# Optimization experiments

Measured on AMD Instinct MI355X. Metric: run time of the kernel, lower is better.

The kernel has to match this reference:

```python
import jax, jax.numpy as jnp
import numpy as np

N_NODES = 100000
N_EDGES = 1600000
NFEAT, NHID, NCLASS = 128, 64, 40
NLAYERS = 4
P = 2.0


def setup_inputs() -> dict:
    key = jax.random.key(0)
    ks = jax.random.split(key, 10)
    x = jax.random.normal(ks[0], (N_NODES, NFEAT), dtype=jnp.float32)
    edge_index = jax.random.randint(ks[1], (2, N_EDGES), 0, N_NODES, dtype=jnp.int32)
    s_in = 1.0 / np.sqrt(NFEAT)
    s_h = 1.0 / np.sqrt(NHID)
    return {
        "x": x,
        "edge_index": edge_index,
        "enc_W": jax.random.normal(ks[2], (NHID, NFEAT), dtype=jnp.float32) * s_in,
        "enc_b": jnp.zeros((NHID,), dtype=jnp.float32),
        "conv_W": jax.random.normal(ks[3], (NHID, NHID), dtype=jnp.float32) * s_h,
        "conv_b": jnp.zeros((NHID,), dtype=jnp.float32),
        "W_skip": jax.random.normal(ks[4], (NHID, NHID), dtype=jnp.float32) * s_h,
        "dec_W": jax.random.normal(ks[5], (NCLASS, NHID), dtype=jnp.float32) * s_h,
        "dec_b": jnp.zeros((NCLASS,), dtype=jnp.float32),
    }


def _gcn_conv(X, W, b, src, dst, n):
    # PyG GCNConv: add self-loops, symmetric normalization, then X @ W^T + b
    H = X @ W.T  # [n, nhid]
    ones = jnp.ones_like(dst, dtype=X.dtype)
    deg = jax.ops.segment_sum(ones, dst, num_segments=n)  # in-degree incl. self loops
    dinv = jnp.where(deg > 0, jax.lax.rsqrt(deg), 0.0)
    norm = dinv[src] * dinv[dst]  # [E+n]
    out = jax.ops.segment_sum(norm[:, None] * H[src], dst, num_segments=n)
    return out + b


def _gamma(X, row, col, n, p):
    # G2 gating: scatter-mean over edges of sum |X[row]-X[col]|^p, then tanh.
    # (conv_gg output in the original G2 is dead code and omitted.)
    diff = jnp.sum(jnp.abs(X[row] - X[col]) ** p, axis=-1)  # [E]
    s = jax.ops.segment_sum(diff, row, num_segments=n)
    cnt = jax.ops.segment_sum(jnp.ones_like(diff), row, num_segments=n)
    return jnp.tanh(s / jnp.maximum(cnt, 1.0))  # [n]


def reference(x, edge_index, enc_W, enc_b, conv_W, conv_b, W_skip, dec_W, dec_b):
    n = x.shape[0]
    row, col = edge_index[0], edge_index[1]
    # self-loop augmented edges for GCNConv
    loop = jnp.arange(n, dtype=edge_index.dtype)
    src_sl = jnp.concatenate([row, loop])
    dst_sl = jnp.concatenate([col, loop])

    X = jax.nn.relu(x @ enc_W.T + enc_b)  # [n, nhid]
    X_init = X
    skip_val = X_init @ W_skip.T  # constant across layers

    for _ in range(NLAYERS):
        X_agg = jax.nn.relu(_gcn_conv(X, conv_W, conv_b, src_sl, dst_sl, n))
        g = _gamma(X, row, col, n, P)[:, None]  # gamma_smooth == gamma_squash (dead convs)
        denom = 1.0 + g + g
        A = 1.0 / denom
        B = g / denom
        C = g / denom
        X = A * X + B * X_agg + C * skip_val

    return X @ dec_W.T + dec_b  # [n, nclass]
```

## Files before the change

### kernel.cpp

```cpp
#include <hip/hip_runtime.h>
#include <hip/hip_bf16.h>

#define NFEAT 128
#define NHID  64
#define NCLASS 40
#define NLAYERS 4


__global__ void count_rank_k(const int* __restrict__ ei, int E,
                             int* __restrict__ cnt_col, int* __restrict__ rank) {
    int t = blockIdx.x * blockDim.x + threadIdx.x;
    int base = t * 4;
    if (base >= E) return;
    if (base + 4 <= E) {
        int4 c4 = *reinterpret_cast<const int4*>(ei + E + base);
        int4 k4;
        k4.x = atomicAdd(&cnt_col[c4.x], 1);
        k4.y = atomicAdd(&cnt_col[c4.y], 1);
        k4.z = atomicAdd(&cnt_col[c4.z], 1);
        k4.w = atomicAdd(&cnt_col[c4.w], 1);
        *reinterpret_cast<int4*>(rank + base) = k4;
    } else {
        for (int e = base; e < E; ++e)
            rank[e] = atomicAdd(&cnt_col[ei[E + e]], 1);
    }
}

__global__ void scanA_k(const int* __restrict__ cnt, int* __restrict__ off,
                        int* __restrict__ bsum, float* __restrict__ dinv, int n) {
    __shared__ int t[1024];
    int i = blockIdx.x * 1024 + threadIdx.x;
    int x = (i < n) ? cnt[i] : 0;
    if (i < n) dinv[i] = 1.0f / sqrtf((float)(x + 1));
    t[threadIdx.x] = x;
    __syncthreads();
    for (int d = 1; d < 1024; d <<= 1) {
        int y = (threadIdx.x >= (unsigned)d) ? t[threadIdx.x - d] : 0;
        __syncthreads();
        t[threadIdx.x] += y;
        __syncthreads();
    }
    if (i < n) off[i] = t[threadIdx.x] - x;
    if (threadIdx.x == 1023) bsum[blockIdx.x] = t[1023];
}

__global__ void scanB_k(int* __restrict__ bsum, int nb) {
    __shared__ int t[1024];
    int x = (threadIdx.x < (unsigned)nb) ? bsum[threadIdx.x] : 0;
    t[threadIdx.x] = x;
    __syncthreads();
    for (int d = 1; d < 1024; d <<= 1) {
        int y = (threadIdx.x >= (unsigned)d) ? t[threadIdx.x - d] : 0;
        __syncthreads();
        t[threadIdx.x] += y;
        __syncthreads();
    }
    if (threadIdx.x < (unsigned)nb) bsum[threadIdx.x] = t[threadIdx.x] - x;
}

__global__ void scanC_k(int* __restrict__ off, const int* __restrict__ bsum,
                        float* __restrict__ gs, int n, int total) {
    int i = blockIdx.x * 1024 + threadIdx.x;
    if (i < n) {
        off[i] += bsum[blockIdx.x];
        gs[i] = 0.f;
    }
    if (i == 0) off[n] = total;
}

__global__ void scatter_k(const int* __restrict__ ei, int E,
                          const int* __restrict__ col_off, const int* __restrict__ rank,
                          int* __restrict__ cnt_row, int* __restrict__ csr) {
    int t = blockIdx.x * blockDim.x + threadIdx.x;
    int base = t * 8;
    if (base >= E) return;
    if (base + 8 <= E) {
        int4 rA = *reinterpret_cast<const int4*>(ei + base);
        int4 rB = *reinterpret_cast<const int4*>(ei + base + 4);
        int4 cA = *reinterpret_cast<const int4*>(ei + E + base);
        int4 cB = *reinterpret_cast<const int4*>(ei + E + base + 4);
        int4 kA = *reinterpret_cast<const int4*>(rank + base);
        int4 kB = *reinterpret_cast<const int4*>(rank + base + 4);
        atomicAdd(&cnt_row[rA.x], 1);
        atomicAdd(&cnt_row[rA.y], 1);
        atomicAdd(&cnt_row[rA.z], 1);
        atomicAdd(&cnt_row[rA.w], 1);
        atomicAdd(&cnt_row[rB.x], 1);
        atomicAdd(&cnt_row[rB.y], 1);
        atomicAdd(&cnt_row[rB.z], 1);
        atomicAdd(&cnt_row[rB.w], 1);
        csr[col_off[cA.x] + kA.x] = rA.x;
        csr[col_off[cA.y] + kA.y] = rA.y;
        csr[col_off[cA.z] + kA.z] = rA.z;
        csr[col_off[cA.w] + kA.w] = rA.w;
        csr[col_off[cB.x] + kB.x] = rB.x;
        csr[col_off[cB.y] + kB.y] = rB.y;
        csr[col_off[cB.z] + kB.z] = rB.z;
        csr[col_off[cB.w] + kB.w] = rB.w;
    } else {
        for (int e = base; e < E; ++e) {
            atomicAdd(&cnt_row[ei[e]], 1);
            csr[col_off[ei[E + e]] + rank[e]] = ei[e];
        }
    }
}


template<int K, int M, bool RELU, bool BIAS>
__global__ void dense_small_k(const float* __restrict__ A, const float* __restrict__ W,
                              const float* __restrict__ b, float* __restrict__ out, int n) {
    int v = blockIdx.x * blockDim.x + threadIdx.x;
    if (v >= n) return;
    float a[K];
    const float4* ap = reinterpret_cast<const float4*>(A + (size_t)v * K);
#pragma unroll
    for (int k = 0; k < K / 4; ++k) {
        float4 t = ap[k];
        a[4 * k + 0] = t.x; a[4 * k + 1] = t.y; a[4 * k + 2] = t.z; a[4 * k + 3] = t.w;
    }
    float4* op = reinterpret_cast<float4*>(out + (size_t)v * M);
#pragma unroll 1
    for (int m = 0; m < M; m += 4) {
        float acc0 = BIAS ? b[m + 0] : 0.f;
        float acc1 = BIAS ? b[m + 1] : 0.f;
        float acc2 = BIAS ? b[m + 2] : 0.f;
        float acc3 = BIAS ? b[m + 3] : 0.f;
#pragma unroll
        for (int k = 0; k < K; ++k) {
            float av = a[k];
            acc0 = fmaf(av, W[(m + 0) * K + k], acc0);
            acc1 = fmaf(av, W[(m + 1) * K + k], acc1);
            acc2 = fmaf(av, W[(m + 2) * K + k], acc2);
            acc3 = fmaf(av, W[(m + 3) * K + k], acc3);
        }
        if (RELU) {
            acc0 = fmaxf(acc0, 0.f); acc1 = fmaxf(acc1, 0.f);
            acc2 = fmaxf(acc2, 0.f); acc3 = fmaxf(acc3, 0.f);
        }
        float4 o; o.x = acc0; o.y = acc1; o.z = acc2; o.w = acc3;
        op[m >> 2] = o;
    }
}


template<int K, int M, int MC>
__global__ void dense_enc_k(const float* __restrict__ A, const float* __restrict__ W,
                            const float* __restrict__ b, float* __restrict__ out, int n) {
    int v = blockIdx.x * blockDim.x + threadIdx.x;
    if (v >= n) return;
    const float4* ap = reinterpret_cast<const float4*>(A + (size_t)v * K);
    float4* op = reinterpret_cast<float4*>(out + (size_t)v * M);
#pragma unroll 1
    for (int mc = 0; mc < M; mc += MC) {
        float acc[MC];
#pragma unroll
        for (int m = 0; m < MC; ++m) acc[m] = b[mc + m];
#pragma unroll 1
        for (int kb = 0; kb < K / 4; ++kb) {
            float4 a4 = ap[kb];
#pragma unroll
            for (int m = 0; m < MC; ++m) {
                const float* wr = W + (size_t)(mc + m) * K + kb * 4;
                acc[m] = fmaf(a4.x, wr[0], acc[m]);
                acc[m] = fmaf(a4.y, wr[1], acc[m]);
                acc[m] = fmaf(a4.z, wr[2], acc[m]);
                acc[m] = fmaf(a4.w, wr[3], acc[m]);
            }
        }
#pragma unroll
        for (int m = 0; m < MC; m += 4) {
            float4 o;
            o.x = fmaxf(acc[m + 0], 0.f);
            o.y = fmaxf(acc[m + 1], 0.f);
            o.z = fmaxf(acc[m + 2], 0.f);
            o.w = fmaxf(acc[m + 3], 0.f);
            op[(mc + m) >> 2] = o;
        }
    }
}

__global__ void gather_k(const float* __restrict__ X, const int* __restrict__ csr,
                         const int* __restrict__ col_off, const float* __restrict__ dinv,
                         float* __restrict__ pre, float* __restrict__ gs, int n) {
    int gid = (blockIdx.x * blockDim.x + threadIdx.x) >> 4;
    int ngrp = (gridDim.x * blockDim.x) >> 4;
    int sub = threadIdx.x & 15;

    for (int v = gid; v < n; v += ngrp) {
        float4 xv = reinterpret_cast<const float4*>(X + (size_t)v * NHID)[sub];
        int beg = col_off[v], end = col_off[v + 1];
        float4 acc = make_float4(0.f, 0.f, 0.f, 0.f);
        int e = beg;
        for (; e + 4 <= end; e += 4) {
            int s0 = csr[e], s1 = csr[e + 1], s2 = csr[e + 2], s3 = csr[e + 3];
            float w0 = dinv[s0], w1 = dinv[s1], w2 = dinv[s2], w3 = dinv[s3];
            float4 x0 = reinterpret_cast<const float4*>(X + (size_t)s0 * NHID)[sub];
            float4 x1 = reinterpret_cast<const float4*>(X + (size_t)s1 * NHID)[sub];
            float4 x2 = reinterpret_cast<const float4*>(X + (size_t)s2 * NHID)[sub];
            float4 x3 = reinterpret_cast<const float4*>(X + (size_t)s3 * NHID)[sub];
            acc.x = fmaf(w0, x0.x, acc.x); acc.y = fmaf(w0, x0.y, acc.y);
            acc.z = fmaf(w0, x0.z, acc.z); acc.w = fmaf(w0, x0.w, acc.w);
            acc.x = fmaf(w1, x1.x, acc.x); acc.y = fmaf(w1, x1.y, acc.y);
            acc.z = fmaf(w1, x1.z, acc.z); acc.w = fmaf(w1, x1.w, acc.w);
            acc.x = fmaf(w2, x2.x, acc.x); acc.y = fmaf(w2, x2.y, acc.y);
            acc.z = fmaf(w2, x2.z, acc.z); acc.w = fmaf(w2, x2.w, acc.w);
            acc.x = fmaf(w3, x3.x, acc.x); acc.y = fmaf(w3, x3.y, acc.y);
            acc.z = fmaf(w3, x3.z, acc.z); acc.w = fmaf(w3, x3.w, acc.w);
            float dx = x0.x - xv.x; float p0 = dx * dx;
            dx = x0.y - xv.y; p0 = fmaf(dx, dx, p0);
            dx = x0.z - xv.z; p0 = fmaf(dx, dx, p0);
            dx = x0.w - xv.w; p0 = fmaf(dx, dx, p0);
            dx = x1.x - xv.x; float p1 = dx * dx;
            dx = x1.y - xv.y; p1 = fmaf(dx, dx, p1);
            dx = x1.z - xv.z; p1 = fmaf(dx, dx, p1);
            dx = x1.w - xv.w; p1 = fmaf(dx, dx, p1);
            dx = x2.x - xv.x; float p2 = dx * dx;
            dx = x2.y - xv.y; p2 = fmaf(dx, dx, p2);
            dx = x2.z - xv.z; p2 = fmaf(dx, dx, p2);
            dx = x2.w - xv.w; p2 = fmaf(dx, dx, p2);
            dx = x3.x - xv.x; float p3 = dx * dx;
            dx = x3.y - xv.y; p3 = fmaf(dx, dx, p3);
            dx = x3.z - xv.z; p3 = fmaf(dx, dx, p3);
            dx = x3.w - xv.w; p3 = fmaf(dx, dx, p3);
#pragma unroll
            for (int m = 1; m <= 8; m <<= 1) {
                p0 += __shfl_xor(p0, m, 64);
                p1 += __shfl_xor(p1, m, 64);
                p2 += __shfl_xor(p2, m, 64);
                p3 += __shfl_xor(p3, m, 64);
            }
            if (sub == 0) {
                atomicAdd(&gs[s0], p0);
                atomicAdd(&gs[s1], p1);
                atomicAdd(&gs[s2], p2);
                atomicAdd(&gs[s3], p3);
            }
        }
        for (; e < end; ++e) {
            int s = csr[e];
            float w = dinv[s];
            float4 xs = reinterpret_cast<const float4*>(X + (size_t)s * NHID)[sub];
            acc.x = fmaf(w, xs.x, acc.x); acc.y = fmaf(w, xs.y, acc.y);
            acc.z = fmaf(w, xs.z, acc.z); acc.w = fmaf(w, xs.w, acc.w);
            float dx = xs.x - xv.x; float part = dx * dx;
            dx = xs.y - xv.y; part = fmaf(dx, dx, part);
            dx = xs.z - xv.z; part = fmaf(dx, dx, part);
            dx = xs.w - xv.w; part = fmaf(dx, dx, part);
#pragma unroll
            for (int m = 1; m <= 8; m <<= 1) part += __shfl_xor(part, m, 64);
            if (sub == 0) atomicAdd(&gs[s], part);
        }
        float dv = dinv[v];
        float dv2 = dv * dv;
        float4 o;
        o.x = fmaf(dv, acc.x, dv2 * xv.x);
        o.y = fmaf(dv, acc.y, dv2 * xv.y);
        o.z = fmaf(dv, acc.z, dv2 * xv.z);
        o.w = fmaf(dv, acc.w, dv2 * xv.w);
        reinterpret_cast<float4*>(pre + (size_t)v * NHID)[sub] = o;
    }
}

__global__ void update_k(float* __restrict__ X, const float* __restrict__ pre,
                         const float* __restrict__ skip, const float* __restrict__ W,
                         const float* __restrict__ b, float* __restrict__ gs,
                         const int* __restrict__ cnt_row, int n) {
    int v = blockIdx.x * blockDim.x + threadIdx.x;
    if (v >= n) return;
    float a[NHID];
    const float4* ap = reinterpret_cast<const float4*>(pre + (size_t)v * NHID);
#pragma unroll
    for (int k = 0; k < NHID / 4; ++k) {
        float4 t = ap[k];
        a[4 * k + 0] = t.x; a[4 * k + 1] = t.y; a[4 * k + 2] = t.z; a[4 * k + 3] = t.w;
    }
    float gv = tanhf(gs[v] / fmaxf((float)cnt_row[v], 1.f));
    gs[v] = 0.f;
    float inv = 1.0f / (1.0f + 2.0f * gv);

    float4* Xp = reinterpret_cast<float4*>(X + (size_t)v * NHID);
    const float4* Sp = reinterpret_cast<const float4*>(skip + (size_t)v * NHID);
#pragma unroll 1
    for (int m = 0; m < NHID; m += 4) {
        float t0 = b[m + 0], t1 = b[m + 1], t2 = b[m + 2], t3 = b[m + 3];
#pragma unroll
        for (int k = 0; k < NHID; ++k) {
            float av = a[k];
            t0 = fmaf(av, W[(m + 0) * NHID + k], t0);
            t1 = fmaf(av, W[(m + 1) * NHID + k], t1);
            t2 = fmaf(av, W[(m + 2) * NHID + k], t2);
            t3 = fmaf(av, W[(m + 3) * NHID + k], t3);
        }
        t0 = fmaxf(t0, 0.f); t1 = fmaxf(t1, 0.f);
        t2 = fmaxf(t2, 0.f); t3 = fmaxf(t3, 0.f);
        float4 x4 = Xp[m >> 2];
        float4 s4 = Sp[m >> 2];
        float4 o;
        o.x = (x4.x + gv * (t0 + s4.x)) * inv;
        o.y = (x4.y + gv * (t1 + s4.y)) * inv;
        o.z = (x4.z + gv * (t2 + s4.z)) * inv;
        o.w = (x4.w + gv * (t3 + s4.w)) * inv;
        Xp[m >> 2] = o;
    }
}


extern "C" void kernel_launch(void* const* d_in, const int* in_sizes, int n_in,
                              void* d_out, int out_size, void* d_ws, size_t ws_size,
                              hipStream_t stream) {
    const float* x      = (const float*)d_in[0];
    const int*   ei     = (const int*)  d_in[1];
    const float* enc_W  = (const float*)d_in[2];
    const float* enc_b  = (const float*)d_in[3];
    const float* conv_W = (const float*)d_in[4];
    const float* conv_b = (const float*)d_in[5];
    const float* W_skip = (const float*)d_in[6];
    const float* dec_W  = (const float*)d_in[7];
    const float* dec_b  = (const float*)d_in[8];

    const int n = in_sizes[0] / NFEAT;
    const int E = in_sizes[1] / 2;

    char* ws = (char*)d_ws;
    auto alloc = [&](size_t bytes) {
        char* p = ws;
        ws += (bytes + 255) & ~(size_t)255;
        return p;
    };

    float* X    = (float*)alloc((size_t)n * NHID * 4);
    float* pre  = (float*)alloc((size_t)n * NHID * 4);
    float* skip = (float*)alloc((size_t)n * NHID * 4);
    float* gs   = (float*)alloc((size_t)n * 4);
    float* dinv = (float*)alloc((size_t)n * 4);
    int* cnt_row = (int*)alloc((size_t)n * 4);
    int* cnt_col = (int*)alloc((size_t)n * 4);
    int* col_off = (int*)alloc((size_t)(n + 1) * 4);
    int* rank    = (int*)alloc((size_t)E * 4);
    int* bsc     = (int*)alloc(1024 * 4);
    int* csr     = (int*)alloc((size_t)E * 4);

    hipMemsetAsync(cnt_row, 0, (size_t)n * 4, stream);
    hipMemsetAsync(cnt_col, 0, (size_t)n * 4, stream);

    count_rank_k<<<(E / 4 + 255) / 256, 256, 0, stream>>>(ei, E, cnt_col, rank);

    int nb = (n + 1023) / 1024;
    scanA_k<<<nb, 1024, 0, stream>>>(cnt_col, col_off, bsc, dinv, n);
    scanB_k<<<1, 1024, 0, stream>>>(bsc, nb);
    scanC_k<<<nb, 1024, 0, stream>>>(col_off, bsc, gs, n, E);
    scatter_k<<<(E / 8 + 255) / 256, 256, 0, stream>>>(ei, E, col_off, rank, cnt_row, csr);

    dense_enc_k<NFEAT, NHID, 32><<<(n + 255) / 256, 256, 0, stream>>>(x, enc_W, enc_b, X, n);
    dense_small_k<NHID, NHID, false, false><<<(n + 255) / 256, 256, 0, stream>>>(X, W_skip, nullptr, skip, n);

    for (int l = 0; l < NLAYERS; ++l) {
        gather_k<<<2048, 256, 0, stream>>>(X, csr, col_off, dinv, pre, gs, n);
        update_k<<<(n + 255) / 256, 256, 0, stream>>>(X, pre, skip, conv_W, conv_b, gs, cnt_row, n);
    }

    dense_small_k<NHID, NCLASS, false, true><<<(n + 255) / 256, 256, 0, stream>>>(X, dec_W, dec_b, (float*)d_out, n);
}
```

Baseline: 994.2 us.

## Gather neighbor features from a bf16 shadow copy and fuse encoder with skip projection

Keeps a bf16 copy of the node features, written by the encoder and update kernels, and has the edge gather read that copy instead of the fp32 rows. This halves the bytes fetched per neighbor in the random-access gather, which is the dominant cost. The gather loop is unrolled to 8 edges, the encoder and skip projection are fused into one kernel, and launch bounds are added to all kernels. The trade-off is bf16 rounding in the aggregation and gamma differences, plus an extra bf16 store per layer.

Result: slower. 1.083 ms (+8.9%).

```diff
diff --git a/kernel.cpp b/kernel.cpp
--- a/kernel.cpp
+++ b/kernel.cpp
@@ -6,8 +6,17 @@
 #define NCLASS 40
 #define NLAYERS 4
 
-
-__global__ void count_rank_k(const int* __restrict__ ei, int E,
+static __device__ __forceinline__ unsigned short f2bf(float f) {
+    unsigned u = __float_as_uint(f);
+    unsigned r = (u + 0x7FFF + ((u >> 16) & 1)) >> 16;
+    return (unsigned short)r;
+}
+static __device__ __forceinline__ float bf2f(unsigned short h) {
+    return __uint_as_float((unsigned)h << 16);
+}
+
+
+__global__ __launch_bounds__(256) void count_rank_k(const int* __restrict__ ei, int E,
                              int* __restrict__ cnt_col, int* __restrict__ rank) {
     int t = blockIdx.x * blockDim.x + threadIdx.x;
     int base = t * 4;
@@ -26,7 +35,7 @@
     }
 }
 
-__global__ void scanA_k(const int* __restrict__ cnt, int* __restrict__ off,
+__global__ __launch_bounds__(1024) void scanA_k(const int* __restrict__ cnt, int* __restrict__ off,
                         int* __restrict__ bsum, float* __restrict__ dinv, int n) {
     __shared__ int t[1024];
     int i = blockIdx.x * 1024 + threadIdx.x;
@@ -44,7 +53,7 @@
     if (threadIdx.x == 1023) bsum[blockIdx.x] = t[1023];
 }
 
-__global__ void scanB_k(int* __restrict__ bsum, int nb) {
+__global__ __launch_bounds__(1024) void scanB_k(int* __restrict__ bsum, int nb) {
     __shared__ int t[1024];
     int x = (threadIdx.x < (unsigned)nb) ? bsum[threadIdx.x] : 0;
     t[threadIdx.x] = x;
@@ -58,7 +67,7 @@
     if (threadIdx.x < (unsigned)nb) bsum[threadIdx.x] = t[threadIdx.x] - x;
 }
 
-__global__ void scanC_k(int* __restrict__ off, const int* __restrict__ bsum,
+__global__ __launch_bounds__(1024) void scanC_k(int* __restrict__ off, const int* __restrict__ bsum,
                         float* __restrict__ gs, int n, int total) {
     int i = blockIdx.x * 1024 + threadIdx.x;
     if (i < n) {
@@ -68,7 +77,7 @@
     if (i == 0) off[n] = total;
 }
 
-__global__ void scatter_k(const int* __restrict__ ei, int E,
+__global__ __launch_bounds__(256) void scatter_k(const int* __restrict__ ei, int E,
                           const int* __restrict__ col_off, const int* __restrict__ rank,
                           int* __restrict__ cnt_row, int* __restrict__ csr) {
     int t = blockIdx.x * blockDim.x + threadIdx.x;
@@ -105,9 +114,69 @@
     }
 }
 
+__global__ __launch_bounds__(256) void enc_skip_k(const float* __restrict__ A,
+                        const float* __restrict__ encW, const float* __restrict__ encb,
+                        const float* __restrict__ Wskip,
+                        float* __restrict__ X, unsigned short* __restrict__ X16,
+                        float* __restrict__ skip, int n) {
+    int v = blockIdx.x * blockDim.x + threadIdx.x;
+    if (v >= n) return;
+    const float4* ap = reinterpret_cast<const float4*>(A + (size_t)v * NFEAT);
+    float4* Xp = reinterpret_cast<float4*>(X + (size_t)v * NHID);
+    ushort4* Hp = reinterpret_cast<ushort4*>(X16 + (size_t)v * NHID);
+    float xs[NHID];
+#pragma unroll 1
+    for (int mc = 0; mc < NHID; mc += 32) {
+        float acc[32];
+#pragma unroll
+        for (int m = 0; m < 32; ++m) acc[m] = encb[mc + m];
+#pragma unroll 1
+        for (int kb = 0; kb < NFEAT / 4; ++kb) {
+            float4 a4 = ap[kb];
+#pragma unroll
+            for (int m = 0; m < 32; ++m) {
+                const float* wr = encW + (size_t)(mc + m) * NFEAT + kb * 4;
+                acc[m] = fmaf(a4.x, wr[0], acc[m]);
+                acc[m] = fmaf(a4.y, wr[1], acc[m]);
+                acc[m] = fmaf(a4.z, wr[2], acc[m]);
+                acc[m] = fmaf(a4.w, wr[3], acc[m]);
+            }
+        }
+#pragma unroll
+        for (int m = 0; m < 32; m += 4) {
+            float4 o;
+            o.x = fmaxf(acc[m + 0], 0.f);
+            o.y = fmaxf(acc[m + 1], 0.f);
+            o.z = fmaxf(acc[m + 2], 0.f);
+            o.w = fmaxf(acc[m + 3], 0.f);
+            xs[mc + m + 0] = o.x; xs[mc + m + 1] = o.y;
+            xs[mc + m + 2] = o.z; xs[mc + m + 3] = o.w;
+            Xp[(mc + m) >> 2] = o;
+            ushort4 h;
+            h.x = f2bf(o.x); h.y = f2bf(o.y); h.z = f2bf(o.z); h.w = f2bf(o.w);
+            Hp[(mc + m) >> 2] = h;
+        }
+    }
+    float4* Sp = reinterpret_cast<float4*>(skip + (size_t)v * NHID);
+#pragma unroll 1
+    for (int m = 0; m < NHID; m += 4) {
+        float s0 = 0.f, s1 = 0.f, s2 = 0.f, s3 = 0.f;
+#pragma unroll
+        for (int k = 0; k < NHID; ++k) {
+            float av = xs[k];
+            s0 = fmaf(av, Wskip[(m + 0) * NHID + k], s0);
+            s1 = fmaf(av, Wskip[(m + 1) * NHID + k], s1);
+            s2 = fmaf(av, Wskip[(m + 2) * NHID + k], s2);
+            s3 = fmaf(av, Wskip[(m + 3) * NHID + k], s3);
+        }
+        float4 o; o.x = s0; o.y = s1; o.z = s2; o.w = s3;
+        Sp[m >> 2] = o;
+    }
+}
+
 
 template<int K, int M, bool RELU, bool BIAS>
-__global__ void dense_small_k(const float* __restrict__ A, const float* __restrict__ W,
+__global__ __launch_bounds__(256) void dense_small_k(const float* __restrict__ A, const float* __restrict__ W,
                               const float* __restrict__ b, float* __restrict__ out, int n) {
     int v = blockIdx.x * blockDim.x + threadIdx.x;
     if (v >= n) return;
@@ -143,112 +212,70 @@
 }
 
 
-template<int K, int M, int MC>
-__global__ void dense_enc_k(const float* __restrict__ A, const float* __restrict__ W,
-                            const float* __restrict__ b, float* __restrict__ out, int n) {
-    int v = blockIdx.x * blockDim.x + threadIdx.x;
-    if (v >= n) return;
-    const float4* ap = reinterpret_cast<const float4*>(A + (size_t)v * K);
-    float4* op = reinterpret_cast<float4*>(out + (size_t)v * M);
-#pragma unroll 1
-    for (int mc = 0; mc < M; mc += MC) {
-        float acc[MC];
-#pragma unroll
-        for (int m = 0; m < MC; ++m) acc[m] = b[mc + m];
-#pragma unroll 1
-        for (int kb = 0; kb < K / 4; ++kb) {
-            float4 a4 = ap[kb];
-#pragma unroll
-            for (int m = 0; m < MC; ++m) {
-                const float* wr = W + (size_t)(mc + m) * K + kb * 4;
-                acc[m] = fmaf(a4.x, wr[0], acc[m]);
-                acc[m] = fmaf(a4.y, wr[1], acc[m]);
-                acc[m] = fmaf(a4.z, wr[2], acc[m]);
-                acc[m] = fmaf(a4.w, wr[3], acc[m]);
-            }
-        }
-#pragma unroll
-        for (int m = 0; m < MC; m += 4) {
-            float4 o;
-            o.x = fmaxf(acc[m + 0], 0.f);
-            o.y = fmaxf(acc[m + 1], 0.f);
-            o.z = fmaxf(acc[m + 2], 0.f);
-            o.w = fmaxf(acc[m + 3], 0.f);
-            op[(mc + m) >> 2] = o;
-        }
-    }
-}
-
-__global__ void gather_k(const float* __restrict__ X, const int* __restrict__ csr,
-                         const int* __restrict__ col_off, const float* __restrict__ dinv,
-                         float* __restrict__ pre, float* __restrict__ gs, int n) {
+#define GLOAD(i) \
+    int s##i = csr[e + i]; \
+    float w##i = dinv[s##i]; \
+    ushort4 h##i = reinterpret_cast<const ushort4*>(X16 + (size_t)s##i * NHID)[sub];
+
+#define GPROC(i) \
+    { float fx = bf2f(h##i.x), fy = bf2f(h##i.y), fz = bf2f(h##i.z), fw = bf2f(h##i.w); \
+      acc.x = fmaf(w##i, fx, acc.x); acc.y = fmaf(w##i, fy, acc.y); \
+      acc.z = fmaf(w##i, fz, acc.z); acc.w = fmaf(w##i, fw, acc.w); \
+      float dx = fx - xv.x; p##i = dx * dx; \
+      dx = fy - xv.y; p##i = fmaf(dx, dx, p##i); \
+      dx = fz - xv.z; p##i = fmaf(dx, dx, p##i); \
+      dx = fw - xv.w; p##i = fmaf(dx, dx, p##i); }
+
+__global__ __launch_bounds__(256) void gather16_k(const unsigned short* __restrict__ X16,
+                          const int* __restrict__ csr,
+                          const int* __restrict__ col_off, const float* __restrict__ dinv,
+                          float* __restrict__ pre, float* __restrict__ gs, int n) {
     int gid = (blockIdx.x * blockDim.x + threadIdx.x) >> 4;
     int ngrp = (gridDim.x * blockDim.x) >> 4;
     int sub = threadIdx.x & 15;
 
     for (int v = gid; v < n; v += ngrp) {
-        float4 xv = reinterpret_cast<const float4*>(X + (size_t)v * NHID)[sub];
+        ushort4 hv = reinterpret_cast<const ushort4*>(X16 + (size_t)v * NHID)[sub];
+        float4 xv;
+        xv.x = bf2f(hv.x); xv.y = bf2f(hv.y); xv.z = bf2f(hv.z); xv.w = bf2f(hv.w);
         int beg = col_off[v], end = col_off[v + 1];
         float4 acc = make_float4(0.f, 0.f, 0.f, 0.f);
         int e = beg;
-        for (; e + 4 <= end; e += 4) {
-            int s0 = csr[e], s1 = csr[e + 1], s2 = csr[e + 2], s3 = csr[e + 3];
-            float w0 = dinv[s0], w1 = dinv[s1], w2 = dinv[s2], w3 = dinv[s3];
-            float4 x0 = reinterpret_cast<const float4*>(X + (size_t)s0 * NHID)[sub];
-            float4 x1 = reinterpret_cast<const float4*>(X + (size_t)s1 * NHID)[sub];
-            float4 x2 = reinterpret_cast<const float4*>(X + (size_t)s2 * NHID)[sub];
-            float4 x3 = reinterpret_cast<const float4*>(X + (size_t)s3 * NHID)[sub];
-            acc.x = fmaf(w0, x0.x, acc.x); acc.y = fmaf(w0, x0.y, acc.y);
-            acc.z = fmaf(w0, x0.z, acc.z); acc.w = fmaf(w0, x0.w, acc.w);
-            acc.x = fmaf(w1, x1.x, acc.x); acc.y = fmaf(w1, x1.y, acc.y);
-            acc.z = fmaf(w1, x1.z, acc.z); acc.w = fmaf(w1, x1.w, acc.w);
-            acc.x = fmaf(w2, x2.x, acc.x); acc.y = fmaf(w2, x2.y, acc.y);
-            acc.z = fmaf(w2, x2.z, acc.z); acc.w = fmaf(w2, x2.w, acc.w);
-            acc.x = fmaf(w3, x3.x, acc.x); acc.y = fmaf(w3, x3.y, acc.y);
-            acc.z = fmaf(w3, x3.z, acc.z); acc.w = fmaf(w3, x3.w, acc.w);
-            float dx = x0.x - xv.x; float p0 = dx * dx;
-            dx = x0.y - xv.y; p0 = fmaf(dx, dx, p0);
-            dx = x0.z - xv.z; p0 = fmaf(dx, dx, p0);
-            dx = x0.w - xv.w; p0 = fmaf(dx, dx, p0);
-            dx = x1.x - xv.x; float p1 = dx * dx;
-            dx = x1.y - xv.y; p1 = fmaf(dx, dx, p1);
-            dx = x1.z - xv.z; p1 = fmaf(dx, dx, p1);
-            dx = x1.w - xv.w; p1 = fmaf(dx, dx, p1);
-            dx = x2.x - xv.x; float p2 = dx * dx;
-            dx = x2.y - xv.y; p2 = fmaf(dx, dx, p2);
-            dx = x2.z - xv.z; p2 = fmaf(dx, dx, p2);
-            dx = x2.w - xv.w; p2 = fmaf(dx, dx, p2);
-            dx = x3.x - xv.x; float p3 = dx * dx;
-            dx = x3.y - xv.y; p3 = fmaf(dx, dx, p3);
-            dx = x3.z - xv.z; p3 = fmaf(dx, dx, p3);
-            dx = x3.w - xv.w; p3 = fmaf(dx, dx, p3);
+        for (; e + 8 <= end; e += 8) {
+            GLOAD(0) GLOAD(1) GLOAD(2) GLOAD(3)
+            GLOAD(4) GLOAD(5) GLOAD(6) GLOAD(7)
+            float p0, p1, p2, p3, p4, p5, p6, p7;
+            GPROC(0) GPROC(1) GPROC(2) GPROC(3)
+            GPROC(4) GPROC(5) GPROC(6) GPROC(7)
 #pragma unroll
             for (int m = 1; m <= 8; m <<= 1) {
                 p0 += __shfl_xor(p0, m, 64);
                 p1 += __shfl_xor(p1, m, 64);
                 p2 += __shfl_xor(p2, m, 64);
                 p3 += __shfl_xor(p3, m, 64);
+                p4 += __shfl_xor(p4, m, 64);
+                p5 += __shfl_xor(p5, m, 64);
+                p6 += __shfl_xor(p6, m, 64);
+                p7 += __shfl_xor(p7, m, 64);
             }
             if (sub == 0) {
                 atomicAdd(&gs[s0], p0);
                 atomicAdd(&gs[s1], p1);
                 atomicAdd(&gs[s2], p2);
                 atomicAdd(&gs[s3], p3);
+                atomicAdd(&gs[s4], p4);
+                atomicAdd(&gs[s5], p5);
+                atomicAdd(&gs[s6], p6);
+                atomicAdd(&gs[s7], p7);
             }
         }
         for (; e < end; ++e) {
-            int s = csr[e];
-            float w = dinv[s];
-            float4 xs = reinterpret_cast<const float4*>(X + (size_t)s * NHID)[sub];
-            acc.x = fmaf(w, xs.x, acc.x); acc.y = fmaf(w, xs.y, acc.y);
-            acc.z = fmaf(w, xs.z, acc.z); acc.w = fmaf(w, xs.w, acc.w);
-            float dx = xs.x - xv.x; float part = dx * dx;
-            dx = xs.y - xv.y; part = fmaf(dx, dx, part);
-            dx = xs.z - xv.z; part = fmaf(dx, dx, part);
-            dx = xs.w - xv.w; part = fmaf(dx, dx, part);
-#pragma unroll
-            for (int m = 1; m <= 8; m <<= 1) part += __shfl_xor(part, m, 64);
-            if (sub == 0) atomicAdd(&gs[s], part);
+            GLOAD(0)
+            float p0;
+            GPROC(0)
+#pragma unroll
+            for (int m = 1; m <= 8; m <<= 1) p0 += __shfl_xor(p0, m, 64);
+            if (sub == 0) atomicAdd(&gs[s0], p0);
         }
         float dv = dinv[v];
         float dv2 = dv * dv;
@@ -261,7 +288,8 @@
     }
 }
 
-__global__ void update_k(float* __restrict__ X, const float* __restrict__ pre,
+__global__ __launch_bounds__(256) void update_k(float* __restrict__ X, unsigned short* __restrict__ X16,
+                         const float* __restrict__ pre,
                          const float* __restrict__ skip, const float* __restrict__ W,
                          const float* __restrict__ b, float* __restrict__ gs,
                          const int* __restrict__ cnt_row, int n) {
@@ -279,6 +307,7 @@
     float inv = 1.0f / (1.0f + 2.0f * gv);
 
     float4* Xp = reinterpret_cast<float4*>(X + (size_t)v * NHID);
+    ushort4* Hp = reinterpret_cast<ushort4*>(X16 + (size_t)v * NHID);
     const float4* Sp = reinterpret_cast<const float4*>(skip + (size_t)v * NHID);
 #pragma unroll 1
     for (int m = 0; m < NHID; m += 4) {
@@ -301,6 +330,9 @@
         o.z = (x4.z + gv * (t2 + s4.z)) * inv;
         o.w = (x4.w + gv * (t3 + s4.w)) * inv;
         Xp[m >> 2] = o;
+        ushort4 h;
+        h.x = f2bf(o.x); h.y = f2bf(o.y); h.z = f2bf(o.z); h.w = f2bf(o.w);
+        Hp[m >> 2] = h;
     }
 }
 
@@ -329,6 +361,7 @@
     };
 
     float* X    = (float*)alloc((size_t)n * NHID * 4);
+    unsigned short* X16 = (unsigned short*)alloc((size_t)n * NHID * 2);
     float* pre  = (float*)alloc((size_t)n * NHID * 4);
     float* skip = (float*)alloc((size_t)n * NHID * 4);
     float* gs   = (float*)alloc((size_t)n * 4);
@@ -351,12 +384,11 @@
     scanC_k<<<nb, 1024, 0, stream>>>(col_off, bsc, gs, n, E);
     scatter_k<<<(E / 8 + 255) / 256, 256, 0, stream>>>(ei, E, col_off, rank, cnt_row, csr);
 
-    dense_enc_k<NFEAT, NHID, 32><<<(n + 255) / 256, 256, 0, stream>>>(x, enc_W, enc_b, X, n);
-    dense_small_k<NHID, NHID, false, false><<<(n + 255) / 256, 256, 0, stream>>>(X, W_skip, nullptr, skip, n);
+    enc_skip_k<<<(n + 255) / 256, 256, 0, stream>>>(x, enc_W, enc_b, W_skip, X, X16, skip, n);
 
     for (int l = 0; l < NLAYERS; ++l) {
-        gather_k<<<2048, 256, 0, stream>>>(X, csr, col_off, dinv, pre, gs, n);
-        update_k<<<(n + 255) / 256, 256, 0, stream>>>(X, pre, skip, conv_W, conv_b, gs, cnt_row, n);
+        gather16_k<<<2048, 256, 0, stream>>>(X16, csr, col_off, dinv, pre, gs, n);
+        update_k<<<(n + 255) / 256, 256, 0, stream>>>(X, X16, pre, skip, conv_W, conv_b, gs, cnt_row, n);
     }
 
     dense_small_k<NHID, NCLASS, false, true><<<(n + 255) / 256, 256, 0, stream>>>(X, dec_W, dec_b, (float*)d_out, n);
```
